# Kernel optimization log

Hardware: AMD Instinct MI355X
Metric: run time of the kernel (lower is better)

## Reference

```python
import jax, jax.numpy as jnp
import numpy as np


def _chord_mask(n):
    # Chord-protocol sparsity: mask[i, i] = 1 and mask[i, (i + 2**j) % n] = 1
    m = np.zeros((n, n), dtype=np.float32)
    idx = np.arange(n)
    m[idx, idx] = 1.0
    for j in range(int(np.log2(n))):
        m[idx, (idx + 2 ** j) % n] = 1.0
    return jnp.asarray(m)


def setup_inputs() -> dict:
    key = jax.random.key(0)
    ks = jax.random.split(key, 8)
    B, n_vec, n_dim = 16, 1024, 64
    n_hidden, n_W, n_class = 32, 10, 10
    data = jax.random.normal(ks[0], (B, n_vec, n_dim), dtype=jnp.float32)
    s1 = 1.0 / np.sqrt(n_dim)
    s2 = 1.0 / np.sqrt(n_hidden)
    s3 = 1.0 / np.sqrt(n_vec * n_dim)
    fW1 = jax.random.uniform(ks[1], (n_W, n_dim, n_hidden), jnp.float32, -s1, s1)
    fb1 = jax.random.uniform(ks[2], (n_W, n_hidden), jnp.float32, -s1, s1)
    fW2 = jax.random.uniform(ks[3], (n_W, n_hidden, n_vec), jnp.float32, -s2, s2)
    fb2 = jax.random.uniform(ks[4], (n_W, n_vec), jnp.float32, -s2, s2)
    final_W = jax.random.uniform(ks[5], (n_vec * n_dim, n_class), jnp.float32, -s3, s3)
    final_b = jax.random.uniform(ks[6], (n_class,), jnp.float32, -s3, s3)
    return {"data": data, "fW1": fW1, "fb1": fb1, "fW2": fW2, "fb2": fb2,
            "final_W": final_W, "final_b": final_b}


def reference(data, fW1, fb1, fW2, fb2, final_W, final_b):
    B, n_vec, n_dim = data.shape
    n_W = fW1.shape[0]
    mask = _chord_mask(n_vec)  # [n_vec, n_vec], static constant
    V = data
    residual = V
    # fs[::-1] -> iterate layers in reverse order
    for i in range(n_W - 1, -1, -1):
        h = jax.nn.gelu(jnp.einsum('bnd,dh->bnh', data, fW1[i]) + fb1[i],
                        approximate=False)
        W = jnp.einsum('bnh,hm->bnm', h, fW2[i]) + fb2[i]  # [B, n_vec, n_vec]
        W = W * mask
        V = jnp.einsum('bnm,bmd->bnd', W, V) + residual
        residual = V  # residual_every=True
    flat = V.reshape(B, n_vec * n_dim)
    return flat @ final_W + final_b
```

## Files before the change

kernel.cpp:

```cpp
#include <hip/hip_runtime.h>

#define BATCH 16
#define NVEC 1024
#define NDIM 64
#define NHID 32
#define NW   10
#define NCLS 10
#define NOFF 11
#define WPAD 12

__global__ __launch_bounds__(256) void k_transpose(
    const float* __restrict__ fW2, float* __restrict__ W2T)
{
    __shared__ float tile[NHID][65];
    const int i = blockIdx.y;
    const int m0 = blockIdx.x * 64;
    const int t = threadIdx.x;
    const int tL = t & 63, wv = t >> 6;

    const float* src = fW2 + (size_t)i * NHID * NVEC;
    #pragma unroll
    for (int jj = 0; jj < 8; ++jj) {
        int j = wv * 8 + jj;
        tile[j][tL] = src[(size_t)j * NVEC + m0 + tL];
    }
    __syncthreads();

    float* dst = W2T + (size_t)i * NVEC * NHID;
    const int j = t & 31, mrow = t >> 5;
    #pragma unroll
    for (int g = 0; g < 8; ++g) {
        int m = g * 8 + mrow;
        dst[(size_t)(m0 + m) * NHID + j] = tile[j][m];
    }
}

__global__ __launch_bounds__(256) void k_weights(
    const float* __restrict__ data,
    const float* __restrict__ fW1,
    const float* __restrict__ fb1,
    const float* __restrict__ W2T,
    const float* __restrict__ fb2,
    float* __restrict__ Wsp)
{
    const int i = blockIdx.y;
    const int nbase = blockIdx.x * 8;
    const int t = threadIdx.x;
    const int b  = t & 15;
    const int jq = (t >> 4) & 3;
    const int nl = t >> 6;
    const int j0 = jq * 8;

    __shared__ float sW1[NDIM * NHID];
    __shared__ float sb1[NHID];
    {
        const float4* w1v = (const float4*)(fW1 + (size_t)i * NDIM * NHID);
        float4* s4 = (float4*)sW1;
        for (int k = t; k < NDIM * NHID / 4; k += 256) s4[k] = w1v[k];
        if (t < NHID) sb1[t] = fb1[i * NHID + t];
    }
    __syncthreads();

    float h[2][8];
    #pragma unroll
    for (int r = 0; r < 2; ++r)
        #pragma unroll
        for (int jj = 0; jj < 8; ++jj) h[r][jj] = sb1[j0 + jj];

    const int n0 = nbase + nl * 2;
    const float4* arow0 = (const float4*)(data + ((size_t)(b * NVEC) + n0) * NDIM);
    const float4* arow1 = (const float4*)(data + ((size_t)(b * NVEC) + n0 + 1) * NDIM);

    #pragma unroll 4
    for (int g = 0; g < 16; ++g) {
        float4 a0 = arow0[g];
        float4 a1 = arow1[g];
        float as0[4] = {a0.x, a0.y, a0.z, a0.w};
        float as1[4] = {a1.x, a1.y, a1.z, a1.w};
        #pragma unroll
        for (int dk = 0; dk < 4; ++dk) {
            const float4* wp = (const float4*)(&sW1[(g * 4 + dk) * NHID + j0]);
            float4 w0 = wp[0], w1 = wp[1];
            const float wf[8] = {w0.x, w0.y, w0.z, w0.w, w1.x, w1.y, w1.z, w1.w};
            #pragma unroll
            for (int jj = 0; jj < 8; ++jj) {
                h[0][jj] += as0[dk] * wf[jj];
                h[1][jj] += as1[dk] * wf[jj];
            }
        }
    }

    #pragma unroll
    for (int r = 0; r < 2; ++r)
        #pragma unroll
        for (int jj = 0; jj < 8; ++jj) {
            float x = h[r][jj];
            h[r][jj] = 0.5f * x * (1.0f + erff(x * 0.70710678118654752f));
        }

    const float* w2t = W2T + (size_t)i * NVEC * NHID;
    const float* b2  = fb2 + (size_t)i * NVEC;
    #pragma unroll
    for (int r = 0; r < 2; ++r) {
        const int n = n0 + r;
        float* wout = Wsp + ((size_t)(i * BATCH + b) * NVEC + n) * WPAD;
        #pragma unroll
        for (int o = 0; o < NOFF; ++o) {
            int off = (o == 0) ? 0 : (1 << (o - 1));
            int m = (n + off) & (NVEC - 1);
            const float4* gp = (const float4*)(w2t + (size_t)m * NHID + j0);
            float4 g0 = gp[0], g1 = gp[1];
            float w = h[r][0] * g0.x + h[r][1] * g0.y + h[r][2] * g0.z + h[r][3] * g0.w
                    + h[r][4] * g1.x + h[r][5] * g1.y + h[r][6] * g1.z + h[r][7] * g1.w;
            w += __shfl_xor(w, 16, 64);
            w += __shfl_xor(w, 32, 64);
            if (jq == (o & 3)) wout[o] = w + b2[m];
        }
    }
}

__global__ __launch_bounds__(1024) void k_chain(
    const float* __restrict__ data,
    const float* __restrict__ Wsp,
    const float* __restrict__ Wf,
    float* __restrict__ part)
{
    const int chunk = blockIdx.x;
    const int b     = blockIdx.y;
    const int d0    = chunk * 4;
    const int n     = threadIdx.x;

    __shared__ float4 bufA[NVEC];
    __shared__ float4 bufB[NVEC];

    bufA[n] = *(const float4*)(data + ((size_t)(b * NVEC) + n) * NDIM + d0);

    const float4* wp = (const float4*)(Wsp + ((size_t)((NW - 1) * BATCH + b) * NVEC + n) * WPAD);
    float4 wa = wp[0], wb4 = wp[1], wc = wp[2];
    __syncthreads();

    float4* cur = bufA;
    float4* nxt = bufB;

    for (int l = 0; l < NW; ++l) {
        float4 na, nb, nc;
        if (l < NW - 1) {
            const float4* wpn = (const float4*)(
                Wsp + ((size_t)((NW - 2 - l) * BATCH + b) * NVEC + n) * WPAD);
            na = wpn[0]; nb = wpn[1]; nc = wpn[2];
        }
        const float wgt[12] = {wa.x, wa.y, wa.z, wa.w,
                               wb4.x, wb4.y, wb4.z, wb4.w,
                               wc.x, wc.y, wc.z, wc.w};
        float4 v0 = cur[n];
        float4 acc;
        acc.x = v0.x + wgt[0] * v0.x;
        acc.y = v0.y + wgt[0] * v0.y;
        acc.z = v0.z + wgt[0] * v0.z;
        acc.w = v0.w + wgt[0] * v0.w;
        #pragma unroll
        for (int o = 1; o < NOFF; ++o) {
            int off = 1 << (o - 1);
            float4 vv = cur[(n + off) & (NVEC - 1)];
            acc.x += wgt[o] * vv.x; acc.y += wgt[o] * vv.y;
            acc.z += wgt[o] * vv.z; acc.w += wgt[o] * vv.w;
        }
        nxt[n] = acc;
        __syncthreads();
        float4* tmp = cur; cur = nxt; nxt = tmp;
        if (l < NW - 1) { wa = na; wb4 = nb; wc = nc; }
    }

    float p[NCLS];
    #pragma unroll
    for (int c = 0; c < NCLS; ++c) p[c] = 0.0f;
    {
        float4 vv = cur[n];
        float vs[4] = {vv.x, vv.y, vv.z, vv.w};
        const float4* wfv = (const float4*)(Wf + ((size_t)(n * NDIM + d0)) * NCLS);
        float wf[40];
        #pragma unroll
        for (int k = 0; k < 10; ++k) {
            float4 u = wfv[k];
            wf[k * 4 + 0] = u.x; wf[k * 4 + 1] = u.y;
            wf[k * 4 + 2] = u.z; wf[k * 4 + 3] = u.w;
        }
        #pragma unroll
        for (int d = 0; d < 4; ++d)
            #pragma unroll
            for (int cls = 0; cls < NCLS; ++cls)
                p[cls] += vs[d] * wf[d * NCLS + cls];
    }

    const int lane = n & 63, wv = n >> 6;
    float* sred = (float*)nxt;
    #pragma unroll
    for (int cls = 0; cls < NCLS; ++cls) {
        float v = p[cls];
        #pragma unroll
        for (int s = 32; s > 0; s >>= 1) v += __shfl_down(v, s, 64);
        if (lane == 0) sred[wv * NCLS + cls] = v;
    }
    __syncthreads();
    if (n < NCLS) {
        float s = 0.0f;
        #pragma unroll
        for (int w = 0; w < 16; ++w) s += sred[w * NCLS + n];
        part[(size_t)(b * 16 + chunk) * NCLS + n] = s;
    }
}

__global__ __launch_bounds__(256) void k_finish(
    const float* __restrict__ part, const float* __restrict__ bias,
    float* __restrict__ out)
{
    int t = threadIdx.x;
    if (t < BATCH * NCLS) {
        int b = t / NCLS, cls = t % NCLS;
        float s = bias[cls];
        #pragma unroll
        for (int ch = 0; ch < 16; ++ch) s += part[(size_t)(b * 16 + ch) * NCLS + cls];
        out[t] = s;
    }
}

extern "C" void kernel_launch(void* const* d_in, const int* in_sizes, int n_in,
                              void* d_out, int out_size, void* d_ws, size_t ws_size,
                              hipStream_t stream) {
    const float* data = (const float*)d_in[0];
    const float* fW1  = (const float*)d_in[1];
    const float* fb1  = (const float*)d_in[2];
    const float* fW2  = (const float*)d_in[3];
    const float* fb2  = (const float*)d_in[4];
    const float* fWf  = (const float*)d_in[5];
    const float* fbf  = (const float*)d_in[6];
    float* out = (float*)d_out;

    float* ws   = (float*)d_ws;
    float* Wsp  = ws;
    float* W2T  = Wsp + (size_t)NW * BATCH * NVEC * WPAD;
    float* part = W2T + (size_t)NW * NVEC * NHID;

    k_transpose<<<dim3(NVEC / 64, NW), 256, 0, stream>>>(fW2, W2T);
    k_weights<<<dim3(NVEC / 8, NW), 256, 0, stream>>>(
        data, fW1, fb1, W2T, fb2, Wsp);
    k_chain<<<dim3(NDIM / 4, BATCH), 1024, 0, stream>>>(data, Wsp, fWf, part);
    k_finish<<<dim3(1), 256, 0, stream>>>(part, fbf, out);
}
```

Before: 130.0 us.

## Give each thread a full hidden vector in weight kernel, drop shuffles and LDS

Reworks k_weights so each thread handles one (batch, row) pair and keeps all 32 hidden units in registers. The old design split hidden units across four lanes and combined them with cross-lane shuffles. W1 is now read directly from global/constant memory instead of being staged in shared memory. The grid halves to 640 blocks. This removes shuffles, LDS traffic and the duplicated offset loads, at the cost of more registers per thread, lower parallelism and uncoalesced 128-byte W2T row reads per thread.

```diff
diff --git a/kernel.cpp b/kernel.cpp
--- a/kernel.cpp
+++ b/kernel.cpp
@@ -35,7 +35,7 @@
     }
 }
 
-__global__ __launch_bounds__(256) void k_weights(
+__global__ __launch_bounds__(256, 1) void k_weights(
     const float* __restrict__ data,
     const float* __restrict__ fW1,
     const float* __restrict__ fb1,
@@ -43,79 +43,54 @@
     const float* __restrict__ fb2,
     float* __restrict__ Wsp)
 {
-    const int i = blockIdx.y;
-    const int nbase = blockIdx.x * 8;
-    const int t = threadIdx.x;
-    const int b  = t & 15;
-    const int jq = (t >> 4) & 3;
-    const int nl = t >> 6;
-    const int j0 = jq * 8;
-
-    __shared__ float sW1[NDIM * NHID];
-    __shared__ float sb1[NHID];
-    {
-        const float4* w1v = (const float4*)(fW1 + (size_t)i * NDIM * NHID);
-        float4* s4 = (float4*)sW1;
-        for (int k = t; k < NDIM * NHID / 4; k += 256) s4[k] = w1v[k];
-        if (t < NHID) sb1[t] = fb1[i * NHID + t];
-    }
-    __syncthreads();
-
-    float h[2][8];
-    #pragma unroll
-    for (int r = 0; r < 2; ++r)
-        #pragma unroll
-        for (int jj = 0; jj < 8; ++jj) h[r][jj] = sb1[j0 + jj];
-
-    const int n0 = nbase + nl * 2;
-    const float4* arow0 = (const float4*)(data + ((size_t)(b * NVEC) + n0) * NDIM);
-    const float4* arow1 = (const float4*)(data + ((size_t)(b * NVEC) + n0 + 1) * NDIM);
-
-    #pragma unroll 4
+    const int i  = blockIdx.y;
+    const int t  = threadIdx.x;
+    const int nl = t & 15;
+    const int b  = t >> 4;
+    const int n  = blockIdx.x * 16 + nl;
+
+    const float* w1 = fW1 + (size_t)i * NDIM * NHID;
+    const float* b1 = fb1 + (size_t)i * NHID;
+    float h[NHID];
+    #pragma unroll
+    for (int j = 0; j < NHID; ++j) h[j] = b1[j];
+
+    const float4* arow = (const float4*)(data + ((size_t)(b * NVEC) + n) * NDIM);
+    #pragma unroll 2
     for (int g = 0; g < 16; ++g) {
-        float4 a0 = arow0[g];
-        float4 a1 = arow1[g];
-        float as0[4] = {a0.x, a0.y, a0.z, a0.w};
-        float as1[4] = {a1.x, a1.y, a1.z, a1.w};
+        float4 a = arow[g];
+        float xs[4] = {a.x, a.y, a.z, a.w};
         #pragma unroll
         for (int dk = 0; dk < 4; ++dk) {
-            const float4* wp = (const float4*)(&sW1[(g * 4 + dk) * NHID + j0]);
-            float4 w0 = wp[0], w1 = wp[1];
-            const float wf[8] = {w0.x, w0.y, w0.z, w0.w, w1.x, w1.y, w1.z, w1.w};
+            float x = xs[dk];
+            const float* wr = w1 + (g * 4 + dk) * NHID;
             #pragma unroll
-            for (int jj = 0; jj < 8; ++jj) {
-                h[0][jj] += as0[dk] * wf[jj];
-                h[1][jj] += as1[dk] * wf[jj];
-            }
-        }
-    }
-
-    #pragma unroll
-    for (int r = 0; r < 2; ++r)
-        #pragma unroll
-        for (int jj = 0; jj < 8; ++jj) {
-            float x = h[r][jj];
-            h[r][jj] = 0.5f * x * (1.0f + erff(x * 0.70710678118654752f));
-        }
+            for (int j = 0; j < NHID; ++j) h[j] += x * wr[j];
+        }
+    }
+
+    #pragma unroll
+    for (int j = 0; j < NHID; ++j) {
+        float x = h[j];
+        h[j] = 0.5f * x * (1.0f + erff(x * 0.70710678118654752f));
+    }
 
     const float* w2t = W2T + (size_t)i * NVEC * NHID;
     const float* b2  = fb2 + (size_t)i * NVEC;
-    #pragma unroll
-    for (int r = 0; r < 2; ++r) {
-        const int n = n0 + r;
-        float* wout = Wsp + ((size_t)(i * BATCH + b) * NVEC + n) * WPAD;
-        #pragma unroll
-        for (int o = 0; o < NOFF; ++o) {
-            int off = (o == 0) ? 0 : (1 << (o - 1));
-            int m = (n + off) & (NVEC - 1);
-            const float4* gp = (const float4*)(w2t + (size_t)m * NHID + j0);
-            float4 g0 = gp[0], g1 = gp[1];
-            float w = h[r][0] * g0.x + h[r][1] * g0.y + h[r][2] * g0.z + h[r][3] * g0.w
-                    + h[r][4] * g1.x + h[r][5] * g1.y + h[r][6] * g1.z + h[r][7] * g1.w;
-            w += __shfl_xor(w, 16, 64);
-            w += __shfl_xor(w, 32, 64);
-            if (jq == (o & 3)) wout[o] = w + b2[m];
-        }
+    float* wout = Wsp + ((size_t)(i * BATCH + b) * NVEC + n) * WPAD;
+    #pragma unroll 1
+    for (int o = 0; o < NOFF; ++o) {
+        int off = (o == 0) ? 0 : (1 << (o - 1));
+        int m = (n + off) & (NVEC - 1);
+        const float4* gp = (const float4*)(w2t + (size_t)m * NHID);
+        float acc = b2[m];
+        #pragma unroll
+        for (int k = 0; k < 8; ++k) {
+            float4 gv = gp[k];
+            acc += h[k * 4 + 0] * gv.x + h[k * 4 + 1] * gv.y
+                 + h[k * 4 + 2] * gv.z + h[k * 4 + 3] * gv.w;
+        }
+        wout[o] = acc;
     }
 }
 
@@ -242,7 +217,7 @@
     float* part = W2T + (size_t)NW * NVEC * NHID;
 
     k_transpose<<<dim3(NVEC / 64, NW), 256, 0, stream>>>(fW2, W2T);
-    k_weights<<<dim3(NVEC / 8, NW), 256, 0, stream>>>(
+    k_weights<<<dim3(NVEC / 16, NW), 256, 0, stream>>>(
         data, fW1, fb1, W2T, fb2, Wsp);
     k_chain<<<dim3(NDIM / 4, BATCH), 1024, 0, stream>>>(data, Wsp, fWf, part);
     k_finish<<<dim3(1), 256, 0, stream>>>(part, fbf, out);
```

Result: slower. 143.0 us (+10.0%).
